# Kernel tuning notes

Hardware: AMD Instinct MI355X
Metric: run time of the kernel (lower is better)

The kernel has to match this reference:

```python
import jax, jax.numpy as jnp
import numpy as np

N_HIDDEN = 2048
D_IN = 64
T_STEPS = 4096
WASHOUT = 200
SPECTRAL_RADIUS = 0.9
RIDGE_LAMBDA = 1e-6


def _scale_to_spectral_radius(W, rho, iters=100):
    # power iteration to estimate the dominant eigenvalue magnitude (spectral radius)
    rng = np.random.default_rng(0)
    v = rng.normal(size=W.shape[0]).astype(np.float64)
    v /= np.linalg.norm(v)
    for _ in range(iters):
        w = W @ v
        nrm = np.linalg.norm(w)
        v = w / nrm
    rad = np.linalg.norm(W @ v)
    return W * (rho / rad)


def setup_inputs() -> dict:
    key = jax.random.key(0)
    k1, k2, k3, k4 = jax.random.split(key, 4)
    u = jax.random.normal(k1, (T_STEPS, D_IN), dtype=jnp.float32)
    y = jax.random.normal(k2, (T_STEPS, 1), dtype=jnp.float32)
    W_in = jax.random.normal(k3, (N_HIDDEN, D_IN), dtype=jnp.float32) * 0.1
    W = np.asarray(jax.random.normal(k4, (N_HIDDEN, N_HIDDEN), dtype=jnp.float32), dtype=np.float64)
    W /= np.sqrt(N_HIDDEN)
    W = _scale_to_spectral_radius(W, SPECTRAL_RADIUS)
    W_res = jnp.asarray(W, dtype=jnp.float32)
    return {"u": u, "y": y, "W_in": W_in, "W_res": W_res, "washout": WASHOUT}


def reference(u, y, W_in, W_res, washout):
    # precompute input drive W_in @ u[t] for all t: [T, N]
    drive = u @ W_in.T
    x0 = jnp.zeros((W_res.shape[0],), dtype=u.dtype)

    def step(x, d):
        x = jnp.tanh(W_res @ x + d)
        return x, x

    _, X = jax.lax.scan(step, x0, drive)  # X: [T, N]
    Xw = X[washout:]                      # [T - washout, N]
    yw = y[washout:]                      # [T - washout, 1]
    A = Xw.T @ Xw + RIDGE_LAMBDA * jnp.eye(Xw.shape[1], dtype=Xw.dtype)
    Wout = jnp.linalg.solve(A, Xw.T @ yw)  # [N, 1]
    return Xw @ Wout                       # [T - washout, 1]
```

## Files before the change

### kernel.cpp

```cpp
#include <hip/hip_runtime.h>
#include <math.h>

#define NH      2048
#define TT      4096
#define DIN     64
#define WASH    200
#define TW      (TT - WASH)
#define LAMBDA  1e-6f

#define SCAN_BLOCKS  64
#define CG_BLOCKS    64
#define CG_ITERS     320

typedef unsigned long long u64;

#define X_OFF      ((size_t)0)
#define DRIVE_OFF  ((size_t)TT * NH)
#define A_OFF      DRIVE_OFF
#define B_OFF      ((size_t)2 * TT * NH)
#define INVD_OFF   (B_OFF + NH)
#define XV_OFF     (INVD_OFF + NH)
#define WS_FLOATS  (XV_OFF + NH)
#define XPACK_OFF  ((size_t)0)
#define ZPACK_OFF  ((size_t)2 * NH)
#define PQSLOT_OFF ((size_t)3 * NH)
#define RZSLOT_OFF ((size_t)3 * NH + 64)
#define U64_TOTAL  ((size_t)3 * NH + 128)

__device__ __forceinline__ u64 pack_ev(int epoch, float v) {
    return ((u64)(unsigned)epoch << 32) | (u64)__float_as_uint(v);
}
__device__ __forceinline__ int   ep_of(u64 p)  { return (int)(p >> 32); }
__device__ __forceinline__ float val_of(u64 p) { return __uint_as_float((unsigned)p); }

__device__ __forceinline__ u64 aload(const u64* p) {
    return __hip_atomic_load(p, __ATOMIC_RELAXED, __HIP_MEMORY_SCOPE_AGENT);
}
__device__ __forceinline__ void astore(u64* p, u64 v) {
    __hip_atomic_store(p, v, __ATOMIC_RELAXED, __HIP_MEMORY_SCOPE_AGENT);
}

__global__ void init_kernel(float* ws) {
    int tid = threadIdx.x;
    u64* ub = (u64*)(ws + WS_FLOATS);
    for (size_t i = tid; i < U64_TOTAL; i += 256) ub[i] = 0ull;
    for (int i = tid; i < NH; i += 256) ws[B_OFF + i] = 0.f;
}

__global__ __launch_bounds__(256) void drive_kernel(
    const float* __restrict__ u, const float* __restrict__ Win,
    float* __restrict__ drive)
{
    __shared__ float Wt[256 * 64];
    const int tid = threadIdx.x;
    const int ic = blockIdx.x & 7;
    const int tc = blockIdx.x >> 3;
    const int i0 = ic * 256;
    for (int idx = tid; idx < 256 * 64; idx += 256) {
        int il = idx >> 6, k = idx & 63;
        Wt[k * 256 + il] = Win[(size_t)i0 * 64 + idx];
    }
    __syncthreads();
    for (int tt_ = 0; tt_ < 128; ++tt_) {
        int t = tc * 128 + tt_;
        const float* ur = u + (size_t)t * DIN;
        float acc = 0.f;
        #pragma unroll
        for (int k = 0; k < 64; ++k)
            acc = fmaf(Wt[k * 256 + tid], ur[k], acc);
        drive[(size_t)t * NH + i0 + tid] = acc;
    }
}

__global__ __launch_bounds__(1024, 1) void scan_kernel(
    const float* __restrict__ W, const float* __restrict__ drive,
    float* __restrict__ X, u64* xpack)
{
    __shared__ float xls[NH];
    const int tid  = threadIdx.x;
    const int wave = tid >> 6;
    const int lane = tid & 63;
    const int rowA = blockIdx.x * 32 + wave * 2;

    float4 wA[8], wB[8];
    {
        const float* wpA = W + (size_t)rowA * NH + lane * 4;
        const float* wpB = wpA + NH;
        #pragma unroll
        for (int j = 0; j < 8; ++j) {
            wA[j] = *(const float4*)(wpA + 256 * j);
            wB[j] = *(const float4*)(wpB + 256 * j);
        }
    }

    for (int t = 0; t < TT; ++t) {
        float dval = (lane < 2) ? drive[(size_t)t * NH + rowA + lane] : 0.f;

        if (t == 0) {
            xls[tid] = 0.f; xls[tid + 1024] = 0.f;
        } else {
            const u64* src = xpack + (size_t)((t - 1) & 1) * NH;
            const int want = t;
            u64 a = aload(&src[tid]);
            u64 b = aload(&src[tid + 1024]);
            bool pa = true, pb = true;
            if (ep_of(a) >= want) { xls[tid] = val_of(a); pa = false; }
            if (ep_of(b) >= want) { xls[tid + 1024] = val_of(b); pb = false; }
            while (pa || pb) {
                __builtin_amdgcn_s_sleep(1);
                if (pa) { u64 v = aload(&src[tid]);
                          if (ep_of(v) >= want) { xls[tid] = val_of(v); pa = false; } }
                if (pb) { u64 v = aload(&src[tid + 1024]);
                          if (ep_of(v) >= want) { xls[tid + 1024] = val_of(v); pb = false; } }
            }
        }
        __syncthreads();

        float a0 = 0.f, a1 = 0.f;
        #pragma unroll
        for (int j = 0; j < 8; ++j) {
            float4 xv = *(const float4*)&xls[lane * 4 + 256 * j];
            float4 va = wA[j], vb = wB[j];
            a0 = fmaf(va.x, xv.x, fmaf(va.y, xv.y, fmaf(va.z, xv.z, fmaf(va.w, xv.w, a0))));
            a1 = fmaf(vb.x, xv.x, fmaf(vb.y, xv.y, fmaf(vb.z, xv.z, fmaf(vb.w, xv.w, a1))));
        }
        #pragma unroll
        for (int m = 32; m; m >>= 1) { a0 += __shfl_xor(a0, m); a1 += __shfl_xor(a1, m); }

        if (lane < 2) {
            float acc = (lane == 0) ? a0 : a1;
            int row = rowA + lane;
            float v = tanhf(acc + dval);
            X[(size_t)t * NH + row] = v;
            astore(&xpack[(size_t)(t & 1) * NH + row], pack_ev(t + 1, v));
        }
        __syncthreads();
    }
}

__global__ __launch_bounds__(256) void gram_kernel(
    const float* __restrict__ X, float* __restrict__ A)
{
    if (blockIdx.x < blockIdx.y) return;
    __shared__ float As[16 * 64];
    __shared__ float Bs[16 * 64];
    const int tx = threadIdx.x, ty = threadIdx.y;
    const int tid = ty * 16 + tx;
    const int i0 = blockIdx.y * 64, j0 = blockIdx.x * 64;
    const int ty4 = ty * 4, tx4 = tx * 4;
    float acc[4][4] = {};

    const int nch = (TW + 15) / 16;
    for (int ch = 0; ch < nch; ++ch) {
        int tbase = WASH + ch * 16;
        for (int v = tid; v < 16 * 64; v += 256) {
            int kk = v >> 6, col = v & 63;
            int t = tbase + kk;
            float a_ = 0.f, b_ = 0.f;
            if (t < TT) {
                a_ = X[(size_t)t * NH + i0 + col];
                b_ = X[(size_t)t * NH + j0 + col];
            }
            As[v] = a_; Bs[v] = b_;
        }
        __syncthreads();
        #pragma unroll
        for (int k = 0; k < 16; ++k) {
            float4 av = *(const float4*)&As[k * 64 + ty4];
            float4 bv = *(const float4*)&Bs[k * 64 + tx4];
            float a[4] = {av.x, av.y, av.z, av.w};
            float b[4] = {bv.x, bv.y, bv.z, bv.w};
            #pragma unroll
            for (int ai = 0; ai < 4; ++ai)
                #pragma unroll
                for (int bi = 0; bi < 4; ++bi)
                    acc[ai][bi] = fmaf(a[ai], b[bi], acc[ai][bi]);
        }
        __syncthreads();
    }
    const bool diag = (blockIdx.x == blockIdx.y);
    #pragma unroll
    for (int ai = 0; ai < 4; ++ai) {
        int gi = i0 + ty4 + ai;
        #pragma unroll
        for (int bi = 0; bi < 4; ++bi) {
            int gj = j0 + tx4 + bi;
            float v = acc[ai][bi];
            if (gi == gj) v += LAMBDA;
            A[(size_t)gi * NH + gj] = v;
            if (!diag) A[(size_t)gj * NH + gi] = v;
        }
    }
}

__global__ void bvec_kernel(const float* __restrict__ X, const float* __restrict__ y,
                            float* __restrict__ bv)
{
    const int ic = blockIdx.x & 7, tc = blockIdx.x >> 3;
    const int i = ic * 256 + threadIdx.x;
    const int t0 = WASH + tc * (TW / 8), t1 = t0 + (TW / 8);
    float acc = 0.f;
    for (int t = t0; t < t1; ++t)
        acc = fmaf(X[(size_t)t * NH + i], y[t], acc);
    atomicAdd(&bv[i], acc);
}

__global__ void invdiag_kernel(const float* __restrict__ A, float* __restrict__ invd)
{
    int i = blockIdx.x * 256 + threadIdx.x;
    invd[i] = 1.0f / A[(size_t)i * NH + i];
}

__global__ __launch_bounds__(1024, 1) void cg_kernel(
    const float* __restrict__ A, const float* __restrict__ bvec,
    const float* __restrict__ invd, float* __restrict__ xv,
    u64* zpack, u64* pqslot, u64* rzslot)
{
    __shared__ float pls[NH];
    __shared__ float zls[NH];
    __shared__ float r32[32], x32[32], q32[32], inv32[32];
    __shared__ float csh[2];
    const int tid     = threadIdx.x;
    const int r_local = tid >> 5;
    const int lane32  = tid & 31;
    const int row0 = blockIdx.x * 32;
    const int row  = row0 + r_local;

    float4 areg[16];
    {
        const float* ap = A + (size_t)row * NH + lane32 * 4;
        #pragma unroll
        for (int j = 0; j < 16; ++j) areg[j] = *(const float4*)(ap + 128 * j);
    }

    pls[tid] = 0.f; pls[tid + 1024] = 0.f;

    if (tid < 32) {
        int i = row0 + tid;
        float bi = bvec[i], iv = invd[i];
        inv32[tid] = iv;
        x32[tid] = 0.f; r32[tid] = bi;
        float zi = iv * bi;
        astore(&zpack[i], pack_ev(1, zi));
        float part = bi * zi;
        #pragma unroll
        for (int m = 16; m; m >>= 1) part += __shfl_xor(part, m, 32);
        if (tid == 0) astore(&rzslot[blockIdx.x], pack_ev(1, part));
    }
    __syncthreads();

    float rho_prev = 1.f;

    for (int it = 0; it < CG_ITERS; ++it) {
        {
            const int want = it + 1;
            u64 a = aload(&zpack[tid]);
            u64 b = aload(&zpack[tid + 1024]);
            bool pa = true, pb = true;
            if (ep_of(a) >= want) { zls[tid] = val_of(a); pa = false; }
            if (ep_of(b) >= want) { zls[tid + 1024] = val_of(b); pb = false; }
            while (pa || pb) {
                __builtin_amdgcn_s_sleep(1);
                if (pa) { u64 v = aload(&zpack[tid]);
                          if (ep_of(v) >= want) { zls[tid] = val_of(v); pa = false; } }
                if (pb) { u64 v = aload(&zpack[tid + 1024]);
                          if (ep_of(v) >= want) { zls[tid + 1024] = val_of(v); pb = false; } }
            }
        }
        if (tid < 64) {
            u64 v = aload(&rzslot[tid]);
            while (ep_of(v) < it + 1) { __builtin_amdgcn_s_sleep(1); v = aload(&rzslot[tid]); }
            float s = val_of(v);
            #pragma unroll
            for (int m = 32; m; m >>= 1) s += __shfl_xor(s, m);
            if (tid == 0) csh[1] = s;
        }
        __syncthreads();
        float rho = csh[1];
        float beta = (it == 0) ? 0.f : ((rho_prev != 0.f) ? rho / rho_prev : 0.f);

        pls[tid]        = fmaf(beta, pls[tid],        zls[tid]);
        pls[tid + 1024] = fmaf(beta, pls[tid + 1024], zls[tid + 1024]);
        __syncthreads();

        float acc = 0.f;
        #pragma unroll
        for (int j = 0; j < 16; ++j) {
            float4 pv = *(const float4*)&pls[lane32 * 4 + 128 * j];
            float4 av = areg[j];
            acc = fmaf(av.x, pv.x, fmaf(av.y, pv.y,
                  fmaf(av.z, pv.z, fmaf(av.w, pv.w, acc))));
        }
        #pragma unroll
        for (int m = 16; m; m >>= 1) acc += __shfl_xor(acc, m, 32);
        if (lane32 == 0) q32[r_local] = acc;
        __syncthreads();

        if (tid < 32) {
            float t1 = q32[tid] * pls[row0 + tid];
            #pragma unroll
            for (int m = 16; m; m >>= 1) t1 += __shfl_xor(t1, m, 32);
            if (tid == 0) astore(&pqslot[blockIdx.x], pack_ev(it + 1, t1));
        }
        if (tid < 64) {
            u64 v = aload(&pqslot[tid]);
            while (ep_of(v) < it + 1) { __builtin_amdgcn_s_sleep(1); v = aload(&pqslot[tid]); }
            float s = val_of(v);
            #pragma unroll
            for (int m = 32; m; m >>= 1) s += __shfl_xor(s, m);
            if (tid == 0) csh[0] = s;
        }
        __syncthreads();
        float pq = csh[0];
        float alpha = (pq != 0.f) ? rho / pq : 0.f;

        if (tid < 32) {
            int i = row0 + tid;
            float pi = pls[i], qi = q32[tid];
            x32[tid] = fmaf(alpha, pi, x32[tid]);
            float ri = r32[tid] - alpha * qi;
            r32[tid] = ri;
            float zi = inv32[tid] * ri;
            astore(&zpack[i], pack_ev(it + 2, zi));
            float t2 = ri * zi;
            #pragma unroll
            for (int m = 16; m; m >>= 1) t2 += __shfl_xor(t2, m, 32);
            if (tid == 0) astore(&rzslot[blockIdx.x], pack_ev(it + 2, t2));
        }
        rho_prev = rho;
        __syncthreads();
    }

    if (tid < 32) xv[row0 + tid] = x32[tid];
}

__global__ void out_kernel(const float* __restrict__ X, const float* __restrict__ w,
                           float* __restrict__ out)
{
    __shared__ float red[4];
    const int tid = threadIdx.x;
    const int rowt = WASH + blockIdx.x;
    float acc = 0.f;
    #pragma unroll
    for (int j = 0; j < 8; ++j) {
        int c = tid + 256 * j;
        acc = fmaf(X[(size_t)rowt * NH + c], w[c], acc);
    }
    #pragma unroll
    for (int m = 32; m; m >>= 1) acc += __shfl_xor(acc, m);
    if ((tid & 63) == 0) red[tid >> 6] = acc;
    __syncthreads();
    if (tid == 0) out[blockIdx.x] = red[0] + red[1] + red[2] + red[3];
}

extern "C" void kernel_launch(void* const* d_in, const int* in_sizes, int n_in,
                              void* d_out, int out_size, void* d_ws, size_t ws_size,
                              hipStream_t stream)
{
    const float* u    = (const float*)d_in[0];
    const float* y    = (const float*)d_in[1];
    const float* Win  = (const float*)d_in[2];
    const float* Wres = (const float*)d_in[3];

    float* ws = (float*)d_ws;
    float* X     = ws + X_OFF;
    float* drive = ws + DRIVE_OFF;
    float* A     = ws + A_OFF;
    u64*   ub    = (u64*)(ws + WS_FLOATS);
    u64*   xpack  = ub + XPACK_OFF;
    u64*   zpack  = ub + ZPACK_OFF;
    u64*   pqslot = ub + PQSLOT_OFF;
    u64*   rzslot = ub + RZSLOT_OFF;

    init_kernel<<<1, 256, 0, stream>>>(ws);
    drive_kernel<<<256, 256, 0, stream>>>(u, Win, drive);
    scan_kernel<<<SCAN_BLOCKS, 1024, 0, stream>>>(Wres, drive, X, xpack);
    gram_kernel<<<dim3(32, 32), dim3(16, 16), 0, stream>>>(X, A);
    bvec_kernel<<<64, 256, 0, stream>>>(X, y, ws + B_OFF);
    invdiag_kernel<<<8, 256, 0, stream>>>(A, ws + INVD_OFF);
    cg_kernel<<<CG_BLOCKS, 1024, 0, stream>>>(A, ws + B_OFF, ws + INVD_OFF,
                                              ws + XV_OFF, zpack, pqslot, rzslot);
    out_kernel<<<TW, 256, 0, stream>>>(X, ws + XV_OFF, (float*)d_out);
}
```

Baseline: 13.32 ms.

## Fuse reservoir scan and Gram accumulation into one persistent overlapped kernel

The sequential scan and the Gram-matrix computation now run in one launch. 64 blocks run the recurrence while 192 worker blocks build Gram tiles over triangular tile indices. The workers poll the epoch-tagged xpack flags and consume 16-step chunks of X as soon as those steps are published, so the X^T X work hides behind the latency-bound scan. Each scan block also packs its two outputs and drive reads into 64-bit accesses, and writes a final epoch marker so the last chunk can be released. The design relies on all 256 blocks being co-resident, and the polling workers add memory traffic that may slow the scan's critical path.

```diff
diff --git a/kernel.cpp b/kernel.cpp
--- a/kernel.cpp
+++ b/kernel.cpp
@@ -8,9 +8,10 @@
 #define TW      (TT - WASH)
 #define LAMBDA  1e-6f
 
-#define SCAN_BLOCKS  64
 #define CG_BLOCKS    64
 #define CG_ITERS     320
+#define NTILE        528
+#define NWORK        192
 
 typedef unsigned long long u64;
 
@@ -32,6 +33,11 @@
 }
 __device__ __forceinline__ int   ep_of(u64 p)  { return (int)(p >> 32); }
 __device__ __forceinline__ float val_of(u64 p) { return __uint_as_float((unsigned)p); }
+__device__ __forceinline__ u64 pack2f(float lo, float hi) {
+    return ((u64)__float_as_uint(hi) << 32) | (u64)__float_as_uint(lo);
+}
+__device__ __forceinline__ float lo_of(u64 p) { return __uint_as_float((unsigned)p); }
+__device__ __forceinline__ float hi_of(u64 p) { return __uint_as_float((unsigned)(p >> 32)); }
 
 __device__ __forceinline__ u64 aload(const u64* p) {
     return __hip_atomic_load(p, __ATOMIC_RELAXED, __HIP_MEMORY_SCOPE_AGENT);
@@ -72,123 +78,154 @@
     }
 }
 
-__global__ __launch_bounds__(1024, 1) void scan_kernel(
+__global__ __launch_bounds__(1024, 1) void scan_gram_kernel(
     const float* __restrict__ W, const float* __restrict__ drive,
-    float* __restrict__ X, u64* xpack)
+    float* __restrict__ X, u64* xpack, float* __restrict__ A)
 {
     __shared__ float xls[NH];
-    const int tid  = threadIdx.x;
-    const int wave = tid >> 6;
-    const int lane = tid & 63;
-    const int rowA = blockIdx.x * 32 + wave * 2;
-
-    float4 wA[8], wB[8];
-    {
-        const float* wpA = W + (size_t)rowA * NH + lane * 4;
-        const float* wpB = wpA + NH;
-        #pragma unroll
-        for (int j = 0; j < 8; ++j) {
-            wA[j] = *(const float4*)(wpA + 256 * j);
-            wB[j] = *(const float4*)(wpB + 256 * j);
-        }
-    }
-
-    for (int t = 0; t < TT; ++t) {
-        float dval = (lane < 2) ? drive[(size_t)t * NH + rowA + lane] : 0.f;
-
-        if (t == 0) {
-            xls[tid] = 0.f; xls[tid + 1024] = 0.f;
-        } else {
-            const u64* src = xpack + (size_t)((t - 1) & 1) * NH;
-            const int want = t;
-            u64 a = aload(&src[tid]);
-            u64 b = aload(&src[tid + 1024]);
-            bool pa = true, pb = true;
-            if (ep_of(a) >= want) { xls[tid] = val_of(a); pa = false; }
-            if (ep_of(b) >= want) { xls[tid + 1024] = val_of(b); pb = false; }
-            while (pa || pb) {
-                __builtin_amdgcn_s_sleep(1);
-                if (pa) { u64 v = aload(&src[tid]);
-                          if (ep_of(v) >= want) { xls[tid] = val_of(v); pa = false; } }
-                if (pb) { u64 v = aload(&src[tid + 1024]);
-                          if (ep_of(v) >= want) { xls[tid + 1024] = val_of(v); pb = false; } }
-            }
-        }
-        __syncthreads();
-
-        float a0 = 0.f, a1 = 0.f;
-        #pragma unroll
-        for (int j = 0; j < 8; ++j) {
-            float4 xv = *(const float4*)&xls[lane * 4 + 256 * j];
-            float4 va = wA[j], vb = wB[j];
-            a0 = fmaf(va.x, xv.x, fmaf(va.y, xv.y, fmaf(va.z, xv.z, fmaf(va.w, xv.w, a0))));
-            a1 = fmaf(vb.x, xv.x, fmaf(vb.y, xv.y, fmaf(vb.z, xv.z, fmaf(vb.w, xv.w, a1))));
-        }
-        #pragma unroll
-        for (int m = 32; m; m >>= 1) { a0 += __shfl_xor(a0, m); a1 += __shfl_xor(a1, m); }
-
-        if (lane < 2) {
-            float acc = (lane == 0) ? a0 : a1;
-            int row = rowA + lane;
-            float v = tanhf(acc + dval);
-            X[(size_t)t * NH + row] = v;
-            astore(&xpack[(size_t)(t & 1) * NH + row], pack_ev(t + 1, v));
-        }
-        __syncthreads();
-    }
-}
-
-__global__ __launch_bounds__(256) void gram_kernel(
-    const float* __restrict__ X, float* __restrict__ A)
-{
-    if (blockIdx.x < blockIdx.y) return;
-    __shared__ float As[16 * 64];
-    __shared__ float Bs[16 * 64];
-    const int tx = threadIdx.x, ty = threadIdx.y;
-    const int tid = ty * 16 + tx;
-    const int i0 = blockIdx.y * 64, j0 = blockIdx.x * 64;
-    const int ty4 = ty * 4, tx4 = tx * 4;
-    float acc[4][4] = {};
-
-    const int nch = (TW + 15) / 16;
-    for (int ch = 0; ch < nch; ++ch) {
-        int tbase = WASH + ch * 16;
-        for (int v = tid; v < 16 * 64; v += 256) {
-            int kk = v >> 6, col = v & 63;
-            int t = tbase + kk;
-            float a_ = 0.f, b_ = 0.f;
-            if (t < TT) {
-                a_ = X[(size_t)t * NH + i0 + col];
-                b_ = X[(size_t)t * NH + j0 + col];
-            }
-            As[v] = a_; Bs[v] = b_;
-        }
-        __syncthreads();
-        #pragma unroll
-        for (int k = 0; k < 16; ++k) {
-            float4 av = *(const float4*)&As[k * 64 + ty4];
-            float4 bv = *(const float4*)&Bs[k * 64 + tx4];
-            float a[4] = {av.x, av.y, av.z, av.w};
-            float b[4] = {bv.x, bv.y, bv.z, bv.w};
-            #pragma unroll
-            for (int ai = 0; ai < 4; ++ai)
+    __shared__ float As[16][64];
+    __shared__ float Bs[16][64];
+    const int tid = threadIdx.x;
+
+    if (blockIdx.x < 64) {
+        const int wave = tid >> 6;
+        const int lane = tid & 63;
+        const int rowA = blockIdx.x * 32 + wave * 2;
+
+        float4 wA[8], wB[8];
+        {
+            const float* wpA = W + (size_t)rowA * NH + lane * 4;
+            const float* wpB = wpA + NH;
+            #pragma unroll
+            for (int j = 0; j < 8; ++j) {
+                wA[j] = *(const float4*)(wpA + 256 * j);
+                wB[j] = *(const float4*)(wpB + 256 * j);
+            }
+        }
+
+        for (int t = 0; t < TT; ++t) {
+            float2 dv = {0.f, 0.f};
+            if (lane == 0) dv = *(const float2*)&drive[(size_t)t * NH + rowA];
+
+            if (t == 0) {
+                xls[tid] = 0.f; xls[tid + 1024] = 0.f;
+            } else {
+                const u64* src = xpack + (size_t)((t - 1) & 1) * NH;
+                const int want = t;
+                u64 a = aload(&src[tid]);
+                u64 b = aload(&src[tid + 1024]);
+                bool pa = true, pb = true;
+                if (ep_of(a) >= want) { xls[tid] = val_of(a); pa = false; }
+                if (ep_of(b) >= want) { xls[tid + 1024] = val_of(b); pb = false; }
+                while (pa || pb) {
+                    __builtin_amdgcn_s_sleep(1);
+                    if (pa) { u64 v = aload(&src[tid]);
+                              if (ep_of(v) >= want) { xls[tid] = val_of(v); pa = false; } }
+                    if (pb) { u64 v = aload(&src[tid + 1024]);
+                              if (ep_of(v) >= want) { xls[tid + 1024] = val_of(v); pb = false; } }
+                }
+            }
+            __syncthreads();
+
+            float a0 = 0.f, a1 = 0.f;
+            #pragma unroll
+            for (int j = 0; j < 8; ++j) {
+                float4 xv = *(const float4*)&xls[lane * 4 + 256 * j];
+                float4 va = wA[j], vb = wB[j];
+                a0 = fmaf(va.x, xv.x, fmaf(va.y, xv.y, fmaf(va.z, xv.z, fmaf(va.w, xv.w, a0))));
+                a1 = fmaf(vb.x, xv.x, fmaf(vb.y, xv.y, fmaf(vb.z, xv.z, fmaf(vb.w, xv.w, a1))));
+            }
+            #pragma unroll
+            for (int m = 32; m; m >>= 1) { a0 += __shfl_xor(a0, m); a1 += __shfl_xor(a1, m); }
+
+            if (lane == 0) {
+                float v0 = tanhf(a0 + dv.x);
+                float v1 = tanhf(a1 + dv.y);
+                astore((u64*)&X[(size_t)t * NH + rowA], pack2f(v0, v1));
+                u64* dst = xpack + (size_t)(t & 1) * NH;
+                astore(&dst[rowA],     pack_ev(t + 1, v0));
+                astore(&dst[rowA + 1], pack_ev(t + 1, v1));
+            }
+            __syncthreads();
+        }
+        __threadfence();
+        if (lane == 0) {
+            u64* dst = xpack + (size_t)(TT & 1) * NH;
+            astore(&dst[rowA],     pack_ev(TT + 1, 0.f));
+            astore(&dst[rowA + 1], pack_ev(TT + 1, 0.f));
+        }
+    } else {
+        const int wid = blockIdx.x - 64;
+        int ti0[3], tj0[3]; int nt = 0;
+        for (int L = wid; L < NTILE; L += NWORK) {
+            int rem = L, a = 0;
+            while (rem >= 32 - a) { rem -= 32 - a; ++a; }
+            ti0[nt] = a * 64; tj0[nt] = (a + rem) * 64; ++nt;
+        }
+        float4 acc4[3] = {};
+        const int ty = tid >> 5, tx = tid & 31;
+        const u64* Xp = (const u64*)X;
+
+        const int nch = (TW + 15) / 16;
+        for (int ch = 0; ch < nch; ++ch) {
+            const int tb = WASH + ch * 16;
+            const int te = (tb + 15 < TT) ? tb + 15 : TT - 1;
+            const int want = te + 2;
+            const u64* buf = xpack + (size_t)((te + 1) & 1) * NH;
+            if (tid < nt * 128) {
+                int tt_ = tid >> 7, local = tid & 127;
+                int base = (local & 64) ? tj0[tt_] : ti0[tt_];
+                int r = base + (local & 63);
+                u64 v = aload(&buf[r]);
+                while (ep_of(v) < want) { __builtin_amdgcn_s_sleep(64); v = aload(&buf[r]); }
+            }
+            __syncthreads();
+
+            for (int tt_ = 0; tt_ < nt; ++tt_) {
+                const int i0 = ti0[tt_], j0 = tj0[tt_];
+                {
+                    int v = tid & 511;
+                    int kk = v >> 5, c2 = v & 31;
+                    int t = tb + kk;
+                    int base = (tid < 512) ? i0 : j0;
+                    float lo = 0.f, hi = 0.f;
+                    if (t < TT) {
+                        u64 w_ = aload(&Xp[((size_t)t * NH + base) / 2 + c2]);
+                        lo = lo_of(w_); hi = hi_of(w_);
+                    }
+                    float* Sh = (tid < 512) ? &As[kk][c2 * 2] : &Bs[kk][c2 * 2];
+                    Sh[0] = lo; Sh[1] = hi;
+                }
+                __syncthreads();
+                float4 a = acc4[tt_];
                 #pragma unroll
-                for (int bi = 0; bi < 4; ++bi)
-                    acc[ai][bi] = fmaf(a[ai], b[bi], acc[ai][bi]);
-        }
-        __syncthreads();
-    }
-    const bool diag = (blockIdx.x == blockIdx.y);
-    #pragma unroll
-    for (int ai = 0; ai < 4; ++ai) {
-        int gi = i0 + ty4 + ai;
-        #pragma unroll
-        for (int bi = 0; bi < 4; ++bi) {
-            int gj = j0 + tx4 + bi;
-            float v = acc[ai][bi];
-            if (gi == gj) v += LAMBDA;
-            A[(size_t)gi * NH + gj] = v;
-            if (!diag) A[(size_t)gj * NH + gi] = v;
+                for (int k = 0; k < 16; ++k) {
+                    float2 av = *(const float2*)&As[k][ty * 2];
+                    float2 bv = *(const float2*)&Bs[k][tx * 2];
+                    a.x = fmaf(av.x, bv.x, a.x); a.y = fmaf(av.x, bv.y, a.y);
+                    a.z = fmaf(av.y, bv.x, a.z); a.w = fmaf(av.y, bv.y, a.w);
+                }
+                acc4[tt_] = a;
+                __syncthreads();
+            }
+        }
+        for (int tt_ = 0; tt_ < nt; ++tt_) {
+            const int i0 = ti0[tt_], j0 = tj0[tt_];
+            const bool diag = (i0 == j0);
+            float4 a = acc4[tt_];
+            float vals[2][2] = {{a.x, a.y}, {a.z, a.w}};
+            #pragma unroll
+            for (int aa = 0; aa < 2; ++aa) {
+                int gi = i0 + ty * 2 + aa;
+                #pragma unroll
+                for (int bb = 0; bb < 2; ++bb) {
+                    int gj = j0 + tx * 2 + bb;
+                    float v = vals[aa][bb];
+                    if (gi == gj) v += LAMBDA;
+                    A[(size_t)gi * NH + gj] = v;
+                    if (!diag) A[(size_t)gj * NH + gi] = v;
+                }
+            }
         }
     }
 }
@@ -374,8 +411,7 @@
 
     init_kernel<<<1, 256, 0, stream>>>(ws);
     drive_kernel<<<256, 256, 0, stream>>>(u, Win, drive);
-    scan_kernel<<<SCAN_BLOCKS, 1024, 0, stream>>>(Wres, drive, X, xpack);
-    gram_kernel<<<dim3(32, 32), dim3(16, 16), 0, stream>>>(X, A);
+    scan_gram_kernel<<<256, 1024, 0, stream>>>(Wres, drive, X, xpack, A);
     bvec_kernel<<<64, 256, 0, stream>>>(X, y, ws + B_OFF);
     invdiag_kernel<<<8, 256, 0, stream>>>(A, ws + INVD_OFF);
     cg_kernel<<<CG_BLOCKS, 1024, 0, stream>>>(A, ws + B_OFF, ws + INVD_OFF,
```

New measurement: 13.37 ms. Within noise of the previous version (+0.3%).
